# Kernel optimization log

Hardware: AMD Instinct MI355X
Metric: run time of the kernel (lower is better)

Reference implementation:

```python
import jax, jax.numpy as jnp
import numpy as np

EMBED, HEADS, LEVELS, POINTS = 256, 8, 3, 4
SPATIAL = np.array([[128, 128], [64, 64], [32, 32]], dtype=np.int64)  # (H, W) per level
B = 2
S = int((SPATIAL[:, 0] * SPATIAL[:, 1]).sum())  # 21504
Q = S  # encoder self-attention: queries == flattened multi-scale features


def grid_sample_bilinear(img, grid):
    """img: [N,C,H,W]; grid: [N,Q,P,2] (x,y) in [-1,1]; bilinear, zeros padding, align_corners=False.
    Returns [N,C,Q,P]."""
    N, C, H, W = img.shape
    _, Qn, Pn, _ = grid.shape
    x = (grid[..., 0] + 1.0) * (W * 0.5) - 0.5
    y = (grid[..., 1] + 1.0) * (H * 0.5) - 0.5
    x0 = jnp.floor(x)
    y0 = jnp.floor(y)
    wx1 = x - x0
    wy1 = y - y0
    x0i = x0.astype(jnp.int32)
    y0i = y0.astype(jnp.int32)
    imgf = img.reshape(N, C, H * W)

    def gather(ix, iy):
        valid = (ix >= 0) & (ix < W) & (iy >= 0) & (iy < H)
        ixc = jnp.clip(ix, 0, W - 1)
        iyc = jnp.clip(iy, 0, H - 1)
        flat = (iyc * W + ixc).reshape(N, -1)  # [N, Q*P]
        v = jax.vmap(lambda im, f: im[:, f])(imgf, flat)  # [N, C, Q*P]
        return jnp.where(valid.reshape(N, 1, -1), v, 0.0)

    w00 = ((1.0 - wx1) * (1.0 - wy1)).reshape(N, 1, -1)
    w01 = (wx1 * (1.0 - wy1)).reshape(N, 1, -1)
    w10 = ((1.0 - wx1) * wy1).reshape(N, 1, -1)
    w11 = (wx1 * wy1).reshape(N, 1, -1)
    out = (gather(x0i, y0i) * w00 + gather(x0i + 1, y0i) * w01
           + gather(x0i, y0i + 1) * w10 + gather(x0i + 1, y0i + 1) * w11)
    return out.reshape(N, C, Qn, Pn)


def msda_forward(hidden_states, encoder_hidden_states, reference_points, shapes_np,
                 sampling_offsets_w, sampling_offsets_b, attention_weights_w, attention_weights_b,
                 value_proj_w, value_proj_b, output_proj_w, output_proj_b):
    Bn, Qn, E = hidden_states.shape
    H, L, P = HEADS, LEVELS, POINTS
    D = E // H
    Sn = encoder_hidden_states.shape[1]
    value = (encoder_hidden_states @ value_proj_w.T + value_proj_b).reshape(Bn, Sn, H, D)
    off = (hidden_states @ sampling_offsets_w.T + sampling_offsets_b).reshape(Bn, Qn, H, L, P, 2)
    aw = hidden_states @ attention_weights_w.T + attention_weights_b
    aw = jax.nn.softmax(aw.reshape(Bn, Qn, H, L * P), axis=-1).reshape(Bn, Qn, H, L, P)
    # offset normalizer is (W, H) per level
    norm = jnp.asarray(np.stack([shapes_np[:, 1], shapes_np[:, 0]], axis=-1), dtype=hidden_states.dtype)
    loc = reference_points[:, :, None, :, None, :] + off / norm[None, None, None, :, None, :]
    grids = 2.0 * loc - 1.0  # [B,Q,H,L,P,2]
    out = jnp.zeros((Bn * H, D, Qn), value.dtype)
    start = 0
    for lvl in range(L):  # small static loop over levels (distinct spatial shapes)
        h, w = int(shapes_np[lvl, 0]), int(shapes_np[lvl, 1])
        val_l = value[:, start:start + h * w].transpose(0, 2, 3, 1).reshape(Bn * H, D, h, w)
        start += h * w
        g = grids[:, :, :, lvl].transpose(0, 2, 1, 3, 4).reshape(Bn * H, Qn, P, 2)
        sampled = grid_sample_bilinear(val_l, g)  # [B*H, D, Q, P]
        w_l = aw[:, :, :, lvl].transpose(0, 2, 1, 3).reshape(Bn * H, 1, Qn, P)
        out = out + (sampled * w_l).sum(-1)
    out = out.reshape(Bn, H * D, Qn).transpose(0, 2, 1)  # [B,Q,E]
    return out @ output_proj_w.T + output_proj_b


def setup_inputs():
    key = jax.random.key(0)
    ks = jax.random.split(key, 11)
    sc = 0.02
    E, H, L, P = EMBED, HEADS, LEVELS, POINTS
    return {
        "hidden_states": jax.random.normal(ks[0], (B, Q, E), jnp.float32),
        "encoder_hidden_states": jax.random.normal(ks[1], (B, S, E), jnp.float32),
        "reference_points": jax.random.uniform(ks[2], (B, Q, L, 2), jnp.float32),
        "spatial_shapes": jnp.asarray(SPATIAL),
        "sampling_offsets_w": jax.random.normal(ks[3], (H * L * P * 2, E), jnp.float32) * sc,
        "sampling_offsets_b": jax.random.normal(ks[4], (H * L * P * 2,), jnp.float32) * sc,
        "attention_weights_w": jax.random.normal(ks[5], (H * L * P, E), jnp.float32) * sc,
        "attention_weights_b": jax.random.normal(ks[6], (H * L * P,), jnp.float32) * sc,
        "value_proj_w": jax.random.normal(ks[7], (E, E), jnp.float32) * sc,
        "value_proj_b": jax.random.normal(ks[8], (E,), jnp.float32) * sc,
        "output_proj_w": jax.random.normal(ks[9], (E, E), jnp.float32) * sc,
        "output_proj_b": jax.random.normal(ks[10], (E,), jnp.float32) * sc,
    }


def reference(hidden_states, encoder_hidden_states, reference_points, spatial_shapes,
              sampling_offsets_w, sampling_offsets_b, attention_weights_w, attention_weights_b,
              value_proj_w, value_proj_b, output_proj_w, output_proj_b):
    shapes_np = np.asarray(spatial_shapes)  # static per-level (H, W)
    return msda_forward(hidden_states, encoder_hidden_states, reference_points, shapes_np,
                        sampling_offsets_w, sampling_offsets_b, attention_weights_w, attention_weights_b,
                        value_proj_w, value_proj_b, output_proj_w, output_proj_b)
```

## Files before the change

### kernel.cpp

```cpp
#include <hip/hip_runtime.h>
#include <hip/hip_bf16.h>

#define EMBED   256
#define HEADS   8
#define LEVELS  3
#define POINTS  4
#define BATCH   2
#define QLEN    21504
#define SLEN    21504
#define MTOT    (BATCH * QLEN)

typedef __attribute__((ext_vector_type(8))) short short8;
typedef __attribute__((ext_vector_type(4))) float f32x4;

__device__ __forceinline__ short f2bf(float x) {
    unsigned u = __builtin_bit_cast(unsigned, x);
    u += 0x7fffu + ((u >> 16) & 1u);
    return (short)(u >> 16);
}
__device__ __forceinline__ float bf_lo(unsigned u) {
    return __builtin_bit_cast(float, u << 16);
}
__device__ __forceinline__ float bf_hi(unsigned u) {
    return __builtin_bit_cast(float, u & 0xffff0000u);
}
__device__ __forceinline__ void async16(const void* g, void* l) {
    __builtin_amdgcn_global_load_lds((const __attribute__((address_space(1))) void*)g,
                                     (__attribute__((address_space(3))) void*)l, 16, 0, 0);
}

__global__ __launch_bounds__(256)
void cvt_bf16_kernel(const float* __restrict__ in, short* __restrict__ out, int n8)
{
    int i = blockIdx.x * 256 + threadIdx.x;
    if (i >= n8) return;
    float4 a = ((const float4*)in)[2 * i];
    float4 b = ((const float4*)in)[2 * i + 1];
    short8 o;
    o[0] = f2bf(a.x); o[1] = f2bf(a.y); o[2] = f2bf(a.z); o[3] = f2bf(a.w);
    o[4] = f2bf(b.x); o[5] = f2bf(b.y); o[6] = f2bf(b.z); o[7] = f2bf(b.w);
    ((short8*)out)[i] = o;
}

__global__ __launch_bounds__(256)
void pack_weights_kernel(const float* __restrict__ vW, const float* __restrict__ oW,
                         const float* __restrict__ soW, const float* __restrict__ awW,
                         const float* __restrict__ soB, const float* __restrict__ awB,
                         short* __restrict__ vWb, short* __restrict__ oWb,
                         short* __restrict__ soawWb, float* __restrict__ soawB)
{
    int i = blockIdx.x * 256 + threadIdx.x;
    if (i < 65536) {
        vWb[i] = f2bf(vW[i]);
    } else if (i < 131072) {
        int j = i - 65536;
        oWb[j] = f2bf(oW[j]);
    } else if (i < 229376) {
        int j = i - 131072;
        int row = j >> 8, k = j & 255;
        float v = (row < 192) ? soW[row * 256 + k]
                 : (row < 288) ? awW[(row - 192) * 256 + k] : 0.f;
        soawWb[j] = f2bf(v);
    } else if (i < 229760) {
        int row = i - 229376;
        soawB[row] = (row < 192) ? soB[row] : (row < 288) ? awB[row - 192] : 0.f;
    }
}

template<bool OUT_BF16>
__global__ __launch_bounds__(256)
void gemm_mfma_kernel(const short* __restrict__ A, const short* __restrict__ Wt,
                      const float* __restrict__ bias, void* __restrict__ Cout, int ldc)
{
    __shared__ short As[128 * 32];
    __shared__ short Bs[128 * 32];
    const int tid  = threadIdx.x;
    const int bm   = blockIdx.y * 128;
    const int bn   = blockIdx.x * 128;
    const int wave = tid >> 6;
    const int lane = tid & 63;
    const int wr   = wave >> 1, wc = wave & 1;
    const int m16  = lane & 15, ko = lane >> 4;
    const int swz  = (m16 >> 1) & 3;

    const int c0 = tid, c1 = tid + 256;
    const int r0 = c0 >> 2, cg0 = (c0 & 3) ^ ((r0 >> 1) & 3);
    const int r1 = c1 >> 2, cg1 = (c1 & 3) ^ ((r1 >> 1) & 3);
    const short* A0 = A  + (size_t)(bm + r0) * 256 + cg0 * 8;
    const short* A1 = A  + (size_t)(bm + r1) * 256 + cg1 * 8;
    const short* B0 = Wt + (size_t)(bn + r0) * 256 + cg0 * 8;
    const short* B1 = Wt + (size_t)(bn + r1) * 256 + cg1 * 8;
    short* const lA0 = As + c0 * 8;
    short* const lA1 = As + c1 * 8;
    short* const lB0 = Bs + c0 * 8;
    short* const lB1 = Bs + c1 * 8;

    int aIdx[4], bIdx[4];
    #pragma unroll
    for (int t = 0; t < 4; ++t) {
        aIdx[t] = (wr * 64 + t * 16 + m16) * 4 + (ko ^ swz);
        bIdx[t] = (wc * 64 + t * 16 + m16) * 4 + (ko ^ swz);
    }
    const short8* Asv = (const short8*)As;
    const short8* Bsv = (const short8*)Bs;

    f32x4 acc[4][4];
    #pragma unroll
    for (int i = 0; i < 4; ++i)
        #pragma unroll
        for (int j = 0; j < 4; ++j) acc[i][j] = (f32x4)0.f;

    for (int k0 = 0; k0 < 256; k0 += 32) {
        async16(A0 + k0, lA0);
        async16(A1 + k0, lA1);
        async16(B0 + k0, lB0);
        async16(B1 + k0, lB1);
        __syncthreads();
        short8 af[4], bfr[4];
        #pragma unroll
        for (int t = 0; t < 4; ++t) { af[t] = Asv[aIdx[t]]; bfr[t] = Bsv[bIdx[t]]; }
        #pragma unroll
        for (int i = 0; i < 4; ++i)
            #pragma unroll
            for (int j = 0; j < 4; ++j)
                acc[i][j] = __builtin_amdgcn_mfma_f32_16x16x32_bf16(af[i], bfr[j], acc[i][j], 0, 0, 0);
        __syncthreads();
    }

    const int rbase = wr * 64 + ko * 4;
    #pragma unroll
    for (int tj = 0; tj < 4; ++tj) {
        const int col = bn + wc * 64 + tj * 16 + m16;
        const float bv = bias[col];
        #pragma unroll
        for (int ti = 0; ti < 4; ++ti) {
            #pragma unroll
            for (int r = 0; r < 4; ++r) {
                const int row = bm + rbase + ti * 16 + r;
                const float v = acc[ti][tj][r] + bv;
                if (OUT_BF16) ((short*)Cout)[(size_t)row * ldc + col] = f2bf(v);
                else          ((float*)Cout)[(size_t)row * ldc + col] = v;
            }
        }
    }
}

__global__ __launch_bounds__(256)
void msda_sample_kernel(const short* __restrict__ value,
                        const float* __restrict__ offaw,
                        const float* __restrict__ ref,
                        short* __restrict__ attn)
{
    __shared__ int prep[64 * 100];

    const int tid = threadIdx.x;
    const int g   = tid >> 2;
    const int sub = tid & 3;
    const int lq  = g >> 3;
    const int h   = g & 7;
    const int bq  = blockIdx.x * 8 + lq;
    const int b   = bq / QLEN;

    {
        const float* awp = offaw + (size_t)bq * 384 + 192 + h * 12;
        float w[12];
        #pragma unroll
        for (int i = 0; i < 12; ++i) w[i] = awp[i];
        float mx = w[0];
        #pragma unroll
        for (int i = 1; i < 12; ++i) mx = fmaxf(mx, w[i]);
        float s = 0.f;
        #pragma unroll
        for (int i = 0; i < 12; ++i) s += __expf(w[i] - mx);
        const float inv = 1.f / s;

        const float* offp = offaw + (size_t)bq * 384 + h * 24;
        const float* refp = ref + (size_t)bq * 6;

        #pragma unroll
        for (int it = 0; it < 3; ++it) {
            const int p  = sub + it * 4;
            const int l  = p >> 2;
            const int Wl = 128 >> l;
            const int st = (l == 0) ? 0 : (l == 1 ? 16384 : 20480);

            const float ox = offp[p * 2 + 0];
            const float oy = offp[p * 2 + 1];
            const float rx = refp[2 * l + 0];
            const float ry = refp[2 * l + 1];
            const float a  = __expf(w[p] - mx) * inv;

            const float x = fmaf(rx, (float)Wl, ox - 0.5f);
            const float y = fmaf(ry, (float)Wl, oy - 0.5f);
            const float x0f = floorf(x), y0f = floorf(y);
            const int   x0  = (int)x0f,  y0  = (int)y0f;
            const float wx1 = x - x0f, wy1 = y - y0f;
            const float wx0 = 1.f - wx1, wy0 = 1.f - wy1;
            const bool vx0 = (unsigned)x0       < (unsigned)Wl;
            const bool vx1 = (unsigned)(x0 + 1) < (unsigned)Wl;
            const bool vy0 = (unsigned)y0       < (unsigned)Wl;
            const bool vy1 = (unsigned)(y0 + 1) < (unsigned)Wl;

            const int r0c = (b * SLEN + st + y0 * Wl + x0) * 32 + h * 4;
            int4 idx; float4 wv;
            idx.x = (vy0 && vx0) ? r0c                : 0;
            idx.y = (vy0 && vx1) ? r0c + 32           : 0;
            idx.z = (vy1 && vx0) ? r0c + Wl * 32      : 0;
            idx.w = (vy1 && vx1) ? r0c + Wl * 32 + 32 : 0;
            wv.x  = (vy0 && vx0) ? wy0 * wx0 * a : 0.f;
            wv.y  = (vy0 && vx1) ? wy0 * wx1 * a : 0.f;
            wv.z  = (vy1 && vx0) ? wy1 * wx0 * a : 0.f;
            wv.w  = (vy1 && vx1) ? wy1 * wx1 * a : 0.f;

            *(int4*)  &prep[g * 100 + p * 8]     = idx;
            *(float4*)&prep[g * 100 + p * 8 + 4] = wv;
        }
    }
    __syncthreads();

    const int4* vp = (const int4*)value;
    float acc[8];
    #pragma unroll
    for (int j = 0; j < 8; ++j) acc[j] = 0.f;

    #pragma unroll
    for (int p = 0; p < 12; ++p) {
        const int4   idx = *(const int4*)  &prep[g * 100 + p * 8];
        const float4 wv  = *(const float4*)&prep[g * 100 + p * 8 + 4];
        const int4 v0 = vp[idx.x + sub];
        const int4 v1 = vp[idx.y + sub];
        const int4 v2 = vp[idx.z + sub];
        const int4 v3 = vp[idx.w + sub];
        #define ACCUM(V, W) \
            acc[0] = fmaf(W, bf_lo((unsigned)V.x), acc[0]); \
            acc[1] = fmaf(W, bf_hi((unsigned)V.x), acc[1]); \
            acc[2] = fmaf(W, bf_lo((unsigned)V.y), acc[2]); \
            acc[3] = fmaf(W, bf_hi((unsigned)V.y), acc[3]); \
            acc[4] = fmaf(W, bf_lo((unsigned)V.z), acc[4]); \
            acc[5] = fmaf(W, bf_hi((unsigned)V.z), acc[5]); \
            acc[6] = fmaf(W, bf_lo((unsigned)V.w), acc[6]); \
            acc[7] = fmaf(W, bf_hi((unsigned)V.w), acc[7]);
        ACCUM(v0, wv.x) ACCUM(v1, wv.y) ACCUM(v2, wv.z) ACCUM(v3, wv.w)
        #undef ACCUM
    }

    int4 o;
    o.x = ((unsigned)(unsigned short)f2bf(acc[1]) << 16) | (unsigned short)f2bf(acc[0]);
    o.y = ((unsigned)(unsigned short)f2bf(acc[3]) << 16) | (unsigned short)f2bf(acc[2]);
    o.z = ((unsigned)(unsigned short)f2bf(acc[5]) << 16) | (unsigned short)f2bf(acc[4]);
    o.w = ((unsigned)(unsigned short)f2bf(acc[7]) << 16) | (unsigned short)f2bf(acc[6]);
    ((int4*)attn)[(size_t)bq * 32 + h * 4 + sub] = o;
}

extern "C" void kernel_launch(void* const* d_in, const int* in_sizes, int n_in,
                              void* d_out, int out_size, void* d_ws, size_t ws_size,
                              hipStream_t stream) {
    const float* hs  = (const float*)d_in[0];
    const float* enc = (const float*)d_in[1];
    const float* rp  = (const float*)d_in[2];
    const float* soW = (const float*)d_in[4];
    const float* soB = (const float*)d_in[5];
    const float* awW = (const float*)d_in[6];
    const float* awB = (const float*)d_in[7];
    const float* vW  = (const float*)d_in[8];
    const float* vB  = (const float*)d_in[9];
    const float* oW  = (const float*)d_in[10];
    const float* oB  = (const float*)d_in[11];
    float* out = (float*)d_out;

    const int M = MTOT;
    const size_t ME = (size_t)M * 256;

    short* encb   = (short*)d_ws;
    short* hsb    = encb + ME;
    short* valb   = hsb + ME;
    float* offaw  = (float*)(valb + ME);
    short* vWb    = (short*)(offaw + (size_t)M * 384);
    short* oWb    = vWb + 65536;
    short* soawWb = oWb + 65536;
    float* soawB  = (float*)(soawWb + 98304);
    short* attnb  = encb;

    dim3 blk(256);
    const int n8 = (int)(ME / 8);
    cvt_bf16_kernel<<<dim3((n8 + 255) / 256), blk, 0, stream>>>(enc, encb, n8);
    cvt_bf16_kernel<<<dim3((n8 + 255) / 256), blk, 0, stream>>>(hs, hsb, n8);
    pack_weights_kernel<<<dim3(898), blk, 0, stream>>>(vW, oW, soW, awW, soB, awB,
                                                       vWb, oWb, soawWb, soawB);
    gemm_mfma_kernel<true><<<dim3(2, M / 128), blk, 0, stream>>>(encb, vWb, vB, valb, 256);
    gemm_mfma_kernel<false><<<dim3(3, M / 128), blk, 0, stream>>>(hsb, soawWb, soawB, offaw, 384);
    msda_sample_kernel<<<dim3(M / 8), blk, 0, stream>>>(valb, offaw, rp, attnb);
    gemm_mfma_kernel<false><<<dim3(2, M / 128), blk, 0, stream>>>(attnb, oWb, oB, out, 256);
}
```

Baseline: 279.9 us.

## Double-buffer GEMM LDS tiles and merge projection GEMMs and conversions into single launches

Rewrites the MFMA GEMM as a shared device body with double-buffered LDS tiles, so the next K-slice is prefetched while the current one feeds the MFMAs and one barrier per step is removed. The value projection and the offset/attention-weight projection run in one combined grid. The two bf16 input conversions are merged into a single kernel. The aim is to cut launch overhead and hide global-load latency, at the cost of doubled LDS per block and a runtime branch on the output type.

After: 276.5 us. Within noise of the previous version (-1.2%).

```diff
diff --git a/kernel.cpp b/kernel.cpp
--- a/kernel.cpp
+++ b/kernel.cpp
@@ -18,28 +18,27 @@
     u += 0x7fffu + ((u >> 16) & 1u);
     return (short)(u >> 16);
 }
-__device__ __forceinline__ float bf_lo(unsigned u) {
-    return __builtin_bit_cast(float, u << 16);
-}
-__device__ __forceinline__ float bf_hi(unsigned u) {
-    return __builtin_bit_cast(float, u & 0xffff0000u);
-}
+__device__ __forceinline__ float bf_lo(unsigned u) { return __builtin_bit_cast(float, u << 16); }
+__device__ __forceinline__ float bf_hi(unsigned u) { return __builtin_bit_cast(float, u & 0xffff0000u); }
 __device__ __forceinline__ void async16(const void* g, void* l) {
     __builtin_amdgcn_global_load_lds((const __attribute__((address_space(1))) void*)g,
                                      (__attribute__((address_space(3))) void*)l, 16, 0, 0);
 }
 
 __global__ __launch_bounds__(256)
-void cvt_bf16_kernel(const float* __restrict__ in, short* __restrict__ out, int n8)
+void cvt2_bf16_kernel(const float* __restrict__ a, short* __restrict__ ao,
+                      const float* __restrict__ b, short* __restrict__ bo, int n8)
 {
     int i = blockIdx.x * 256 + threadIdx.x;
-    if (i >= n8) return;
-    float4 a = ((const float4*)in)[2 * i];
-    float4 b = ((const float4*)in)[2 * i + 1];
+    const float* src; short* dst; int j;
+    if (i < n8)          { src = a; dst = ao; j = i; }
+    else                 { src = b; dst = bo; j = i - n8; }
+    float4 x = ((const float4*)src)[2 * j];
+    float4 y = ((const float4*)src)[2 * j + 1];
     short8 o;
-    o[0] = f2bf(a.x); o[1] = f2bf(a.y); o[2] = f2bf(a.z); o[3] = f2bf(a.w);
-    o[4] = f2bf(b.x); o[5] = f2bf(b.y); o[6] = f2bf(b.z); o[7] = f2bf(b.w);
-    ((short8*)out)[i] = o;
+    o[0] = f2bf(x.x); o[1] = f2bf(x.y); o[2] = f2bf(x.z); o[3] = f2bf(x.w);
+    o[4] = f2bf(y.x); o[5] = f2bf(y.y); o[6] = f2bf(y.z); o[7] = f2bf(y.w);
+    ((short8*)dst)[j] = o;
 }
 
 __global__ __launch_bounds__(256)
@@ -67,16 +66,13 @@
     }
 }
 
-template<bool OUT_BF16>
-__global__ __launch_bounds__(256)
-void gemm_mfma_kernel(const short* __restrict__ A, const short* __restrict__ Wt,
-                      const float* __restrict__ bias, void* __restrict__ Cout, int ldc)
-{
-    __shared__ short As[128 * 32];
-    __shared__ short Bs[128 * 32];
+__device__ __forceinline__
+void gemm_body(const short* __restrict__ A, const short* __restrict__ Wt,
+               const float* __restrict__ bias, void* __restrict__ Cout,
+               int ldc, bool out_bf16, int bm, int bn,
+               short* __restrict__ As, short* __restrict__ Bs)
+{
     const int tid  = threadIdx.x;
-    const int bm   = blockIdx.y * 128;
-    const int bn   = blockIdx.x * 128;
     const int wave = tid >> 6;
     const int lane = tid & 63;
     const int wr   = wave >> 1, wc = wave & 1;
@@ -90,10 +86,6 @@
     const short* A1 = A  + (size_t)(bm + r1) * 256 + cg1 * 8;
     const short* B0 = Wt + (size_t)(bn + r0) * 256 + cg0 * 8;
     const short* B1 = Wt + (size_t)(bn + r1) * 256 + cg1 * 8;
-    short* const lA0 = As + c0 * 8;
-    short* const lA1 = As + c1 * 8;
-    short* const lB0 = Bs + c0 * 8;
-    short* const lB1 = Bs + c1 * 8;
 
     int aIdx[4], bIdx[4];
     #pragma unroll
@@ -101,8 +93,6 @@
         aIdx[t] = (wr * 64 + t * 16 + m16) * 4 + (ko ^ swz);
         bIdx[t] = (wc * 64 + t * 16 + m16) * 4 + (ko ^ swz);
     }
-    const short8* Asv = (const short8*)As;
-    const short8* Bsv = (const short8*)Bs;
 
     f32x4 acc[4][4];
     #pragma unroll
@@ -110,21 +100,33 @@
         #pragma unroll
         for (int j = 0; j < 4; ++j) acc[i][j] = (f32x4)0.f;
 
-    for (int k0 = 0; k0 < 256; k0 += 32) {
-        async16(A0 + k0, lA0);
-        async16(A1 + k0, lA1);
-        async16(B0 + k0, lB0);
-        async16(B1 + k0, lB1);
+    async16(A0, As + c0 * 8);
+    async16(A1, As + c1 * 8);
+    async16(B0, Bs + c0 * 8);
+    async16(B1, Bs + c1 * 8);
+
+    #pragma unroll
+    for (int kt = 0; kt < 8; ++kt) {
         __syncthreads();
+        if (kt + 1 < 8) {
+            const int nb = (kt + 1) & 1;
+            const int kofs = (kt + 1) * 32;
+            async16(A0 + kofs, As + nb * 4096 + c0 * 8);
+            async16(A1 + kofs, As + nb * 4096 + c1 * 8);
+            async16(B0 + kofs, Bs + nb * 4096 + c0 * 8);
+            async16(B1 + kofs, Bs + nb * 4096 + c1 * 8);
+        }
+        const int ofs = (kt & 1) * 512;
+        const short8* Asv = (const short8*)As;
+        const short8* Bsv = (const short8*)Bs;
         short8 af[4], bfr[4];
         #pragma unroll
-        for (int t = 0; t < 4; ++t) { af[t] = Asv[aIdx[t]]; bfr[t] = Bsv[bIdx[t]]; }
+        for (int t = 0; t < 4; ++t) { af[t] = Asv[ofs + aIdx[t]]; bfr[t] = Bsv[ofs + bIdx[t]]; }
         #pragma unroll
         for (int i = 0; i < 4; ++i)
             #pragma unroll
             for (int j = 0; j < 4; ++j)
                 acc[i][j] = __builtin_amdgcn_mfma_f32_16x16x32_bf16(af[i], bfr[j], acc[i][j], 0, 0, 0);
-        __syncthreads();
     }
 
     const int rbase = wr * 64 + ko * 4;
@@ -138,11 +140,36 @@
             for (int r = 0; r < 4; ++r) {
                 const int row = bm + rbase + ti * 16 + r;
                 const float v = acc[ti][tj][r] + bv;
-                if (OUT_BF16) ((short*)Cout)[(size_t)row * ldc + col] = f2bf(v);
+                if (out_bf16) ((short*)Cout)[(size_t)row * ldc + col] = f2bf(v);
                 else          ((float*)Cout)[(size_t)row * ldc + col] = v;
             }
         }
     }
+}
+
+__global__ __launch_bounds__(256)
+void proj_gemm_kernel(const short* __restrict__ encb, const short* __restrict__ vWb,
+                      const float* __restrict__ vB, short* __restrict__ valb,
+                      const short* __restrict__ hsb, const short* __restrict__ soawWb,
+                      const float* __restrict__ soawB, float* __restrict__ offaw)
+{
+    __shared__ short As[2 * 4096];
+    __shared__ short Bs[2 * 4096];
+    const int bm = blockIdx.y * 128;
+    if (blockIdx.x < 2) {
+        gemm_body(encb, vWb, vB, valb, 256, true, bm, blockIdx.x * 128, As, Bs);
+    } else {
+        gemm_body(hsb, soawWb, soawB, offaw, 384, false, bm, (blockIdx.x - 2) * 128, As, Bs);
+    }
+}
+
+__global__ __launch_bounds__(256)
+void out_gemm_kernel(const short* __restrict__ A, const short* __restrict__ Wt,
+                     const float* __restrict__ bias, float* __restrict__ C)
+{
+    __shared__ short As[2 * 4096];
+    __shared__ short Bs[2 * 4096];
+    gemm_body(A, Wt, bias, C, 256, false, blockIdx.y * 128, blockIdx.x * 128, As, Bs);
 }
 
 __global__ __launch_bounds__(256)
@@ -283,12 +310,11 @@
 
     dim3 blk(256);
     const int n8 = (int)(ME / 8);
-    cvt_bf16_kernel<<<dim3((n8 + 255) / 256), blk, 0, stream>>>(enc, encb, n8);
-    cvt_bf16_kernel<<<dim3((n8 + 255) / 256), blk, 0, stream>>>(hs, hsb, n8);
+    cvt2_bf16_kernel<<<dim3(2 * n8 / 256), blk, 0, stream>>>(enc, encb, hs, hsb, n8);
     pack_weights_kernel<<<dim3(898), blk, 0, stream>>>(vW, oW, soW, awW, soB, awB,
                                                        vWb, oWb, soawWb, soawB);
-    gemm_mfma_kernel<true><<<dim3(2, M / 128), blk, 0, stream>>>(encb, vWb, vB, valb, 256);
-    gemm_mfma_kernel<false><<<dim3(3, M / 128), blk, 0, stream>>>(hsb, soawWb, soawB, offaw, 384);
+    proj_gemm_kernel<<<dim3(5, M / 128), blk, 0, stream>>>(encb, vWb, vB, valb,
+                                                           hsb, soawWb, soawB, offaw);
     msda_sample_kernel<<<dim3(M / 8), blk, 0, stream>>>(valb, offaw, rp, attnb);
-    gemm_mfma_kernel<false><<<dim3(2, M / 128), blk, 0, stream>>>(attnb, oWb, oB, out, 256);
-}
+    out_gemm_kernel<<<dim3(2, M / 128), blk, 0, stream>>>(attnb, oWb, oB, out);
+}
```

## Fuse fp32-to-bf16 conversion into streaming GEMMs and merge projection launches

Applied to the files above, without the earlier changes.

Removes the separate bf16 conversion kernels for the encoder and query inputs. The projection GEMM now reads fp32 activations directly into registers and converts them there. The value and offset/attention projections are merged into one launch, and all GEMMs are restructured so each block keeps a full 128x256 weight tile in LDS (64 KB) while each wave holds its A row strip in registers over the whole K=256. This saves writing and re-reading bf16 copies of the activations. In exchange, each block streams its A rows exactly once but reloads the weight tile, and the larger LDS footprint lowers occupancy.

Measured after the change: 266.2 us. 1.05x faster.

```diff
diff --git a/kernel.cpp b/kernel.cpp
--- a/kernel.cpp
+++ b/kernel.cpp
@@ -18,28 +18,11 @@
     u += 0x7fffu + ((u >> 16) & 1u);
     return (short)(u >> 16);
 }
-__device__ __forceinline__ float bf_lo(unsigned u) {
-    return __builtin_bit_cast(float, u << 16);
-}
-__device__ __forceinline__ float bf_hi(unsigned u) {
-    return __builtin_bit_cast(float, u & 0xffff0000u);
-}
+__device__ __forceinline__ float bf_lo(unsigned u) { return __builtin_bit_cast(float, u << 16); }
+__device__ __forceinline__ float bf_hi(unsigned u) { return __builtin_bit_cast(float, u & 0xffff0000u); }
 __device__ __forceinline__ void async16(const void* g, void* l) {
     __builtin_amdgcn_global_load_lds((const __attribute__((address_space(1))) void*)g,
                                      (__attribute__((address_space(3))) void*)l, 16, 0, 0);
-}
-
-__global__ __launch_bounds__(256)
-void cvt_bf16_kernel(const float* __restrict__ in, short* __restrict__ out, int n8)
-{
-    int i = blockIdx.x * 256 + threadIdx.x;
-    if (i >= n8) return;
-    float4 a = ((const float4*)in)[2 * i];
-    float4 b = ((const float4*)in)[2 * i + 1];
-    short8 o;
-    o[0] = f2bf(a.x); o[1] = f2bf(a.y); o[2] = f2bf(a.z); o[3] = f2bf(a.w);
-    o[4] = f2bf(b.x); o[5] = f2bf(b.y); o[6] = f2bf(b.z); o[7] = f2bf(b.w);
-    ((short8*)out)[i] = o;
 }
 
 __global__ __launch_bounds__(256)
@@ -67,82 +50,93 @@
     }
 }
 
-template<bool OUT_BF16>
-__global__ __launch_bounds__(256)
-void gemm_mfma_kernel(const short* __restrict__ A, const short* __restrict__ Wt,
-                      const float* __restrict__ bias, void* __restrict__ Cout, int ldc)
-{
-    __shared__ short As[128 * 32];
-    __shared__ short Bs[128 * 32];
+template<bool A_FP32, bool OUT_BF16>
+__device__ __forceinline__
+void stream_gemm(const void* __restrict__ Aptr, const short* __restrict__ Wt,
+                 const float* __restrict__ bias, void* __restrict__ Cout,
+                 int ldc, int colbase, int rowstrip, short* __restrict__ Ws)
+{
     const int tid  = threadIdx.x;
-    const int bm   = blockIdx.y * 128;
-    const int bn   = blockIdx.x * 128;
-    const int wave = tid >> 6;
     const int lane = tid & 63;
-    const int wr   = wave >> 1, wc = wave & 1;
-    const int m16  = lane & 15, ko = lane >> 4;
-    const int swz  = (m16 >> 1) & 3;
-
-    const int c0 = tid, c1 = tid + 256;
-    const int r0 = c0 >> 2, cg0 = (c0 & 3) ^ ((r0 >> 1) & 3);
-    const int r1 = c1 >> 2, cg1 = (c1 & 3) ^ ((r1 >> 1) & 3);
-    const short* A0 = A  + (size_t)(bm + r0) * 256 + cg0 * 8;
-    const short* A1 = A  + (size_t)(bm + r1) * 256 + cg1 * 8;
-    const short* B0 = Wt + (size_t)(bn + r0) * 256 + cg0 * 8;
-    const short* B1 = Wt + (size_t)(bn + r1) * 256 + cg1 * 8;
-    short* const lA0 = As + c0 * 8;
-    short* const lA1 = As + c1 * 8;
-    short* const lB0 = Bs + c0 * 8;
-    short* const lB1 = Bs + c1 * 8;
-
-    int aIdx[4], bIdx[4];
-    #pragma unroll
-    for (int t = 0; t < 4; ++t) {
-        aIdx[t] = (wr * 64 + t * 16 + m16) * 4 + (ko ^ swz);
-        bIdx[t] = (wc * 64 + t * 16 + m16) * 4 + (ko ^ swz);
-    }
-    const short8* Asv = (const short8*)As;
-    const short8* Bsv = (const short8*)Bs;
-
-    f32x4 acc[4][4];
-    #pragma unroll
-    for (int i = 0; i < 4; ++i)
-        #pragma unroll
-        for (int j = 0; j < 4; ++j) acc[i][j] = (f32x4)0.f;
-
-    for (int k0 = 0; k0 < 256; k0 += 32) {
-        async16(A0 + k0, lA0);
-        async16(A1 + k0, lA1);
-        async16(B0 + k0, lB0);
-        async16(B1 + k0, lB1);
-        __syncthreads();
-        short8 af[4], bfr[4];
-        #pragma unroll
-        for (int t = 0; t < 4; ++t) { af[t] = Asv[aIdx[t]]; bfr[t] = Bsv[bIdx[t]]; }
-        #pragma unroll
-        for (int i = 0; i < 4; ++i)
-            #pragma unroll
-            for (int j = 0; j < 4; ++j)
-                acc[i][j] = __builtin_amdgcn_mfma_f32_16x16x32_bf16(af[i], bfr[j], acc[i][j], 0, 0, 0);
-        __syncthreads();
-    }
-
-    const int rbase = wr * 64 + ko * 4;
-    #pragma unroll
-    for (int tj = 0; tj < 4; ++tj) {
-        const int col = bn + wc * 64 + tj * 16 + m16;
+    const int wv   = tid >> 6;
+    const int m16  = lane & 15;
+    const int ko   = lane >> 4;
+
+    #pragma unroll
+    for (int i = 0; i < 16; ++i) {
+        const int c    = i * 256 + tid;
+        const int colL = c >> 5;
+        const int cw   = c & 31;
+        const int csw  = (cw & 24) | ((cw ^ colL) & 7);
+        async16(Wt + (((size_t)(colbase + colL)) << 8) + csw * 8, Ws + c * 8);
+    }
+
+    const int row = rowstrip + wv * 16 + m16;
+    short8 afr[8];
+    if (A_FP32) {
+        const float* Af = (const float*)Aptr + (size_t)row * 256 + ko * 8;
+        #pragma unroll
+        for (int kt = 0; kt < 8; ++kt) {
+            float4 x = *(const float4*)(Af + kt * 32);
+            float4 y = *(const float4*)(Af + kt * 32 + 4);
+            short8 t;
+            t[0] = f2bf(x.x); t[1] = f2bf(x.y); t[2] = f2bf(x.z); t[3] = f2bf(x.w);
+            t[4] = f2bf(y.x); t[5] = f2bf(y.y); t[6] = f2bf(y.z); t[7] = f2bf(y.w);
+            afr[kt] = t;
+        }
+    } else {
+        const short* Ab = (const short*)Aptr + (size_t)row * 256 + ko * 8;
+        #pragma unroll
+        for (int kt = 0; kt < 8; ++kt) afr[kt] = *(const short8*)(Ab + kt * 32);
+    }
+
+    __syncthreads();
+
+    const short8* Wvp = (const short8*)Ws;
+    const int r0 = rowstrip + wv * 16 + ko * 4;
+    #pragma unroll
+    for (int ct = 0; ct < 8; ++ct) {
+        const int colL = ct * 16 + m16;
+        const int rowc = colL * 32;
+        f32x4 a = (f32x4)0.f;
+        #pragma unroll
+        for (int kt = 0; kt < 8; ++kt) {
+            const int g = kt * 4 + ko;
+            const int s = (g & 24) | ((g ^ colL) & 7);
+            a = __builtin_amdgcn_mfma_f32_16x16x32_bf16(afr[kt], Wvp[rowc + s], a, 0, 0, 0);
+        }
+        const int col = colbase + colL;
         const float bv = bias[col];
         #pragma unroll
-        for (int ti = 0; ti < 4; ++ti) {
-            #pragma unroll
-            for (int r = 0; r < 4; ++r) {
-                const int row = bm + rbase + ti * 16 + r;
-                const float v = acc[ti][tj][r] + bv;
-                if (OUT_BF16) ((short*)Cout)[(size_t)row * ldc + col] = f2bf(v);
-                else          ((float*)Cout)[(size_t)row * ldc + col] = v;
-            }
-        }
-    }
+        for (int r = 0; r < 4; ++r) {
+            const float v = a[r] + bv;
+            if (OUT_BF16) ((short*)Cout)[(size_t)(r0 + r) * ldc + col] = f2bf(v);
+            else          ((float*)Cout)[(size_t)(r0 + r) * ldc + col] = v;
+        }
+    }
+}
+
+__global__ __launch_bounds__(256)
+void proj_gemm_kernel(const float* __restrict__ enc, const short* __restrict__ vWb,
+                      const float* __restrict__ vB, short* __restrict__ valb,
+                      const float* __restrict__ hs, const short* __restrict__ soawWb,
+                      const float* __restrict__ soawB, float* __restrict__ offaw)
+{
+    __shared__ short Ws[128 * 256];
+    const int rowstrip = blockIdx.y * 64;
+    if (blockIdx.x < 2) {
+        stream_gemm<true, true>(enc, vWb, vB, valb, 256, blockIdx.x * 128, rowstrip, Ws);
+    } else {
+        stream_gemm<true, false>(hs, soawWb, soawB, offaw, 384, (blockIdx.x - 2) * 128, rowstrip, Ws);
+    }
+}
+
+__global__ __launch_bounds__(256)
+void out_gemm_kernel(const short* __restrict__ A, const short* __restrict__ oWb,
+                     const float* __restrict__ oB, float* __restrict__ C)
+{
+    __shared__ short Ws[128 * 256];
+    stream_gemm<false, false>(A, oWb, oB, C, 256, blockIdx.x * 128, blockIdx.y * 64, Ws);
 }
 
 __global__ __launch_bounds__(256)
@@ -202,18 +196,18 @@
             const bool vy1 = (unsigned)(y0 + 1) < (unsigned)Wl;
 
             const int r0c = (b * SLEN + st + y0 * Wl + x0) * 32 + h * 4;
-            int4 idx; float4 wv;
+            int4 idx; float4 wvv;
             idx.x = (vy0 && vx0) ? r0c                : 0;
             idx.y = (vy0 && vx1) ? r0c + 32           : 0;
             idx.z = (vy1 && vx0) ? r0c + Wl * 32      : 0;
             idx.w = (vy1 && vx1) ? r0c + Wl * 32 + 32 : 0;
-            wv.x  = (vy0 && vx0) ? wy0 * wx0 * a : 0.f;
-            wv.y  = (vy0 && vx1) ? wy0 * wx1 * a : 0.f;
-            wv.z  = (vy1 && vx0) ? wy1 * wx0 * a : 0.f;
-            wv.w  = (vy1 && vx1) ? wy1 * wx1 * a : 0.f;
+            wvv.x = (vy0 && vx0) ? wy0 * wx0 * a : 0.f;
+            wvv.y = (vy0 && vx1) ? wy0 * wx1 * a : 0.f;
+            wvv.z = (vy1 && vx0) ? wy1 * wx0 * a : 0.f;
+            wvv.w = (vy1 && vx1) ? wy1 * wx1 * a : 0.f;
 
             *(int4*)  &prep[g * 100 + p * 8]     = idx;
-            *(float4*)&prep[g * 100 + p * 8 + 4] = wv;
+            *(float4*)&prep[g * 100 + p * 8 + 4] = wvv;
         }
     }
     __syncthreads();
@@ -226,7 +220,7 @@
     #pragma unroll
     for (int p = 0; p < 12; ++p) {
         const int4   idx = *(const int4*)  &prep[g * 100 + p * 8];
-        const float4 wv  = *(const float4*)&prep[g * 100 + p * 8 + 4];
+        const float4 wvv = *(const float4*)&prep[g * 100 + p * 8 + 4];
         const int4 v0 = vp[idx.x + sub];
         const int4 v1 = vp[idx.y + sub];
         const int4 v2 = vp[idx.z + sub];
@@ -240,7 +234,7 @@
             acc[5] = fmaf(W, bf_hi((unsigned)V.z), acc[5]); \
             acc[6] = fmaf(W, bf_lo((unsigned)V.w), acc[6]); \
             acc[7] = fmaf(W, bf_hi((unsigned)V.w), acc[7]);
-        ACCUM(v0, wv.x) ACCUM(v1, wv.y) ACCUM(v2, wv.z) ACCUM(v3, wv.w)
+        ACCUM(v0, wvv.x) ACCUM(v1, wvv.y) ACCUM(v2, wvv.z) ACCUM(v3, wvv.w)
         #undef ACCUM
     }
 
@@ -271,24 +265,19 @@
     const int M = MTOT;
     const size_t ME = (size_t)M * 256;
 
-    short* encb   = (short*)d_ws;
-    short* hsb    = encb + ME;
-    short* valb   = hsb + ME;
-    float* offaw  = (float*)(valb + ME);
+    short* valb   = (short*)d_ws;
+    short* attnb  = valb + ME;
+    float* offaw  = (float*)(attnb + ME);
     short* vWb    = (short*)(offaw + (size_t)M * 384);
     short* oWb    = vWb + 65536;
     short* soawWb = oWb + 65536;
     float* soawB  = (float*)(soawWb + 98304);
-    short* attnb  = encb;
 
     dim3 blk(256);
-    const int n8 = (int)(ME / 8);
-    cvt_bf16_kernel<<<dim3((n8 + 255) / 256), blk, 0, stream>>>(enc, encb, n8);
-    cvt_bf16_kernel<<<dim3((n8 + 255) / 256), blk, 0, stream>>>(hs, hsb, n8);
     pack_weights_kernel<<<dim3(898), blk, 0, stream>>>(vW, oW, soW, awW, soB, awB,
                                                        vWb, oWb, soawWb, soawB);
-    gemm_mfma_kernel<true><<<dim3(2, M / 128), blk, 0, stream>>>(encb, vWb, vB, valb, 256);
-    gemm_mfma_kernel<false><<<dim3(3, M / 128), blk, 0, stream>>>(hsb, soawWb, soawB, offaw, 384);
+    proj_gemm_kernel<<<dim3(5, M / 64), blk, 0, stream>>>(enc, vWb, vB, valb,
+                                                          hs, soawWb, soawB, offaw);
     msda_sample_kernel<<<dim3(M / 8), blk, 0, stream>>>(valb, offaw, rp, attnb);
-    gemm_mfma_kernel<false><<<dim3(2, M / 128), blk, 0, stream>>>(attnb, oWb, oB, out, 256);
-}
+    out_gemm_kernel<<<dim3(2, M / 64), blk, 0, stream>>>(attnb, oWb, oB, out);
+}
```
